# Kernel optimization log

Hardware: AMD Instinct MI355X
Metric: run time of the kernel (lower is better)

The kernel has to match this reference:

```python
import jax, jax.numpy as jnp
import numpy as np
import math

K_HEADS = 16  # nb_heads from init_kwargs


def setup_inputs() -> dict:
    key = jax.random.key(0)
    ks = jax.random.split(key, 7)
    B, M, H, D = 2, 2048, 1024, 1024 // K_HEADS
    return {
        "h": jax.random.normal(ks[0], (B, M, H), jnp.float32),
        "h_cache": jax.random.normal(ks[1], (B, M, H), jnp.float32),
        "key_pe": jax.random.normal(ks[2], (1, D, M), jnp.float32),
        "Wq": jax.random.normal(ks[3], (H, H), jnp.float32) * 0.02,
        "Wk": jax.random.normal(ks[4], (H, H), jnp.float32) * 0.02,
        "Wv": jax.random.normal(ks[5], (H, H), jnp.float32) * 0.02,
        "Wo": jax.random.normal(ks[6], (H, H), jnp.float32) * 0.02,
    }


def _heads(x, K):
    # [B, M, H] -> [B, K, M, D]
    B, M, H = x.shape
    return x.reshape(B, M, K, H // K).transpose(0, 2, 1, 3)


def reference(h, h_cache, key_pe, Wq, Wk, Wv, Wo):
    B, M, H = h.shape
    K = K_HEADS
    D = H // K
    q = _heads(h @ Wq.T, K)        # [B, K, M, D]
    k = _heads(h_cache @ Wk.T, K)  # [B, K, L, D], L == M
    v = _heads(h_cache @ Wv.T, K)  # [B, K, L, D]

    attn_cont = jnp.einsum("bkmd,bkld->bkml", q, k)            # content scores
    attn_pos = jnp.einsum("bkmd,dl->bkml", q, key_pe[0])       # positional scores
    attn = (attn_cont + attn_pos[..., :M]) / math.sqrt(D)
    attn = jax.nn.softmax(attn, axis=-1)  # computed as in source, but source
    # (faithfully) multiplies VALUE by attn_cont, not attn:
    out = jnp.einsum("bkml,bkld->bkmd", attn_cont, v)          # [B, K, M, D]
    out = out.transpose(0, 2, 1, 3).reshape(B, M, H)
    return out @ Wo.T
```

## Files before the change

### kernel.cpp

```cpp
#include <hip/hip_runtime.h>
#include <hip/hip_bf16.h>

#define BB 2
#define MM 2048
#define HH 1024
#define KH 16

typedef short s16x8 __attribute__((ext_vector_type(8)));
typedef float f32x4 __attribute__((ext_vector_type(4)));
typedef float f32x16 __attribute__((ext_vector_type(16)));

#define GLOBAL_AS __attribute__((address_space(1)))
#define LDS_AS    __attribute__((address_space(3)))

__device__ __forceinline__ void async_copy16(const void* g, void* l) {
    __builtin_amdgcn_global_load_lds((const GLOBAL_AS void*)g, (LDS_AS void*)l, 16, 0, 0);
}

struct __align__(8) bf16x4_t { __hip_bfloat16 x, y, z, w; };

__global__ __launch_bounds__(256) void cvt_all(
    const float* __restrict__ h_f, const float* __restrict__ hc_f,
    const float* __restrict__ Wk_f, const float* __restrict__ Wv_f,
    const float* __restrict__ Wo_f, const float* __restrict__ Wq_f,
    __hip_bfloat16* __restrict__ hb, __hip_bfloat16* __restrict__ hcT,
    __hip_bfloat16* __restrict__ wkb, __hip_bfloat16* __restrict__ wvb,
    __hip_bfloat16* __restrict__ wob, __hip_bfloat16* __restrict__ wqt,
    float* __restrict__ Sz)
{
    __shared__ float Tl[64][65];
    const int seg = blockIdx.y;
    const int t = threadIdx.x;
    const int bx = blockIdx.x;

    if (seg == 1) {
        if (bx >= BB * 512) return;
        const int b = bx >> 9;
        const int tile = bx & 511;
        const int m0 = (tile >> 4) * 64;
        const int k0 = (tile & 15) * 64;
        const int r = t >> 6;
        const int c = t & 63;
        const float* src = hc_f + (size_t)b * MM * HH;
#pragma unroll
        for (int i = 0; i < 64; i += 4)
            Tl[r + i][c] = src[(size_t)(m0 + r + i) * HH + k0 + c];
        __syncthreads();
        __hip_bfloat16* dst = hcT + (size_t)b * HH * MM;
        const int ml = (t & 15) * 4;
#pragma unroll
        for (int ii = 0; ii < 4; ++ii) {
            const int kl = (t >> 4) + 16 * ii;
            bf16x4_t o;
            o.x = __float2bfloat16(Tl[ml + 0][kl]);
            o.y = __float2bfloat16(Tl[ml + 1][kl]);
            o.z = __float2bfloat16(Tl[ml + 2][kl]);
            o.w = __float2bfloat16(Tl[ml + 3][kl]);
            *(bf16x4_t*)(dst + (size_t)(k0 + kl) * MM + m0 + ml) = o;
        }
        return;
    }
    if (seg == 5) {
        if (bx < 128) {
            const int i = (bx * 256 + t) * 4;
            float4 z = {0.f, 0.f, 0.f, 0.f};
            *(float4*)(Sz + i) = z;
            return;
        }
        if (bx >= 384) return;
        const int tile = bx - 128;
        const int j0 = (tile >> 4) * 64;
        const int k0 = (tile & 15) * 64;
        const int r = t >> 6;
        const int c = t & 63;
#pragma unroll
        for (int i = 0; i < 64; i += 4)
            Tl[r + i][c] = Wq_f[(size_t)(j0 + r + i) * HH + k0 + c];
        __syncthreads();
        const int ml = (t & 15) * 4;
#pragma unroll
        for (int ii = 0; ii < 4; ++ii) {
            const int kl = (t >> 4) + 16 * ii;
            bf16x4_t o;
            o.x = __float2bfloat16(Tl[ml + 0][kl]);
            o.y = __float2bfloat16(Tl[ml + 1][kl]);
            o.z = __float2bfloat16(Tl[ml + 2][kl]);
            o.w = __float2bfloat16(Tl[ml + 3][kl]);
            *(bf16x4_t*)(wqt + (size_t)(k0 + kl) * HH + j0 + ml) = o;
        }
        return;
    }
    const float* src;
    __hip_bfloat16* dst;
    int n;
    switch (seg) {
        case 0: src = h_f;  dst = hb;  n = BB * MM * HH; break;
        case 2: src = Wk_f; dst = wkb; n = HH * HH; break;
        case 3: src = Wv_f; dst = wvb; n = HH * HH; break;
        default: src = Wo_f; dst = wob; n = HH * HH; break;
    }
    const int i = (bx * 256 + t) * 4;
    if (i + 3 < n) {
        const float4 v = *(const float4*)(src + i);
        bf16x4_t o;
        o.x = __float2bfloat16(v.x);
        o.y = __float2bfloat16(v.y);
        o.z = __float2bfloat16(v.z);
        o.w = __float2bfloat16(v.w);
        *(bf16x4_t*)(dst + i) = o;
    }
}

__device__ __forceinline__ void store_c(__hip_bfloat16* C, size_t idx, float v) {
    C[idx] = __float2bfloat16(v);
}
__device__ __forceinline__ void store_c(float* C, size_t idx, float v) { C[idx] = v; }

__device__ __forceinline__ f32x16 nt64_acc(
    const __hip_bfloat16* __restrict__ A, const __hip_bfloat16* __restrict__ B,
    int kd, size_t ld, __hip_bfloat16* As, __hip_bfloat16* Bs)
{
    const int t    = threadIdx.x;
    const int lane = t & 63;
    const int wave = t >> 6;
    const int srow = lane >> 3;
    const int sw   = ((lane & 7) ^ srow) * 8;
    const int wm   = (wave >> 1) * 32;
    const int wn   = (wave & 1) * 32;
    const int fm   = lane & 31;
    const int fm7  = fm & 7;
    const int ghi  = lane >> 5;

    f32x16 acc = {};
    for (int k0 = 0; k0 < kd; k0 += 64) {
        __syncthreads();
#pragma unroll
        for (int i = 0; i < 2; ++i) {
            const int c = wave * 2 + i;
            async_copy16(A + (size_t)(c * 8 + srow) * ld + k0 + sw, As + c * 512);
            async_copy16(B + (size_t)(c * 8 + srow) * ld + k0 + sw, Bs + c * 512);
        }
        __syncthreads();
#pragma unroll
        for (int ks = 0; ks < 64; ks += 16) {
            const int pos = ((((ks >> 3) + ghi) ^ fm7) * 8);
            const s16x8 af = *(const s16x8*)(As + (wm + fm) * 64 + pos);
            const s16x8 bf = *(const s16x8*)(Bs + (wn + fm) * 64 + pos);
            acc = __builtin_amdgcn_mfma_f32_32x32x16_bf16(af, bf, acc, 0, 0, 0);
        }
    }
    return acc;
}

template <typename OutT>
__device__ __forceinline__ void store_tile64(OutT* C, int ldc, const f32x16& acc) {
    const int lane = threadIdx.x & 63;
    const int wave = threadIdx.x >> 6;
    const int wm = (wave >> 1) * 32;
    const int wn = (wave & 1) * 32;
    const int col = wn + (lane & 31);
    const int rb  = 4 * (lane >> 5);
#pragma unroll
    for (int r = 0; r < 16; ++r) {
        const int row = wm + (r & 3) + 8 * (r >> 2) + rb;
        store_c(C, (size_t)row * ldc + col, acc[r]);
    }
}

__global__ __launch_bounds__(256) void gemm_g(
    const __hip_bfloat16* __restrict__ hcT, __hip_bfloat16* __restrict__ G)
{
    __shared__ __align__(16) __hip_bfloat16 As[64 * 64];
    __shared__ __align__(16) __hip_bfloat16 Bs[64 * 64];
    const int b = blockIdx.z;
    const int m0 = blockIdx.x * 64, n0 = blockIdx.y * 64;
    const __hip_bfloat16* Ab = hcT + (size_t)b * HH * MM;
    f32x16 acc = nt64_acc(Ab + (size_t)m0 * MM, Ab + (size_t)n0 * MM, MM, MM, As, Bs);
    store_tile64(G + (size_t)b * HH * HH + (size_t)m0 * HH + n0, HH, acc);
}

#define LPP 72

__global__ __launch_bounds__(256) void gemm_vt(
    const __hip_bfloat16* __restrict__ wkb, const __hip_bfloat16* __restrict__ wvb,
    const __hip_bfloat16* __restrict__ G, float* __restrict__ S)
{
    __shared__ __align__(16) char smem[64 * LPP * 2 + 64 * 64 * 2];
    __hip_bfloat16* As = (__hip_bfloat16*)smem;
    __hip_bfloat16* Bs = (__hip_bfloat16*)(smem + 8192);
    __hip_bfloat16* Pl = (__hip_bfloat16*)smem;
    __hip_bfloat16* Wl = (__hip_bfloat16*)(smem + 64 * LPP * 2);

    const int t    = threadIdx.x;
    const int lane = t & 63;
    const int wave = t >> 6;
    const int kt   = blockIdx.x;
    const int head = blockIdx.y;
    const int b    = blockIdx.z;

    const __hip_bfloat16* Arow = G + (size_t)b * HH * HH + (size_t)kt * 64 * HH;
    const __hip_bfloat16* Brow = wkb + (size_t)head * 64 * HH;

    f32x16 acc = nt64_acc(Arow, Brow, HH, HH, As, Bs);
    __syncthreads();

    {
        const int wm = (wave >> 1) * 32;
        const int wn = (wave & 1) * 32;
        const int col_i = wn + (lane & 31);
        const int ghi4  = 4 * (lane >> 5);
#pragma unroll
        for (int g = 0; g < 4; ++g) {
            const int ccb = wm + 8 * g + ghi4;
            bf16x4_t o;
            o.x = __float2bfloat16(acc[4 * g + 0]);
            o.y = __float2bfloat16(acc[4 * g + 1]);
            o.z = __float2bfloat16(acc[4 * g + 2]);
            o.w = __float2bfloat16(acc[4 * g + 3]);
            *(bf16x4_t*)(Pl + col_i * LPP + ccb) = o;
        }
    }
    {
        const int srow = lane >> 3;
        const int sw   = ((lane & 7) ^ srow) * 8;
#pragma unroll
        for (int i = 0; i < 2; ++i) {
            const int c = wave * 2 + i;
            async_copy16(wvb + (size_t)(head * 64 + c * 8 + srow) * HH + kt * 64 + sw,
                         Wl + c * 512);
        }
    }
    __syncthreads();

    const int fr  = lane & 15;
    const int fq  = (lane >> 4) * 8;
    const int wm2 = wave * 16;

    f32x4 acc2[4] = {};
#pragma unroll
    for (int kk = 0; kk < 64; kk += 32) {
        const s16x8 af = *(const s16x8*)(Pl + (wm2 + fr) * LPP + kk + fq);
#pragma unroll
        for (int nj = 0; nj < 4; ++nj) {
            const int row = nj * 16 + fr;
            const s16x8 bfv = *(const s16x8*)(
                Wl + row * 64 + ((((kk + fq) >> 3) ^ (row & 7)) << 3));
            acc2[nj] = __builtin_amdgcn_mfma_f32_16x16x32_bf16(af, bfv, acc2[nj], 0, 0, 0);
        }
    }

    float* Sg = S + ((size_t)b * KH + head) * 4096;
    const int er = (lane >> 4) * 4;
    const int ec = lane & 15;
#pragma unroll
    for (int nj = 0; nj < 4; ++nj)
#pragma unroll
        for (int rr = 0; rr < 4; ++rr)
            atomicAdd(&Sg[(wm2 + er + rr) * 64 + nj * 16 + ec], acc2[nj][rr]);
}

__global__ __launch_bounds__(256) void gemm_f(
    const __hip_bfloat16* __restrict__ W2, const __hip_bfloat16* __restrict__ WqT,
    __hip_bfloat16* __restrict__ F)
{
    __shared__ __align__(16) __hip_bfloat16 As[64 * 64];
    __shared__ __align__(16) __hip_bfloat16 Bs[64 * 64];
    const int b = blockIdx.z;
    const int m0 = blockIdx.x * 64, n0 = blockIdx.y * 64;
    f32x16 acc = nt64_acc(W2 + (size_t)b * HH * HH + (size_t)m0 * HH,
                          WqT + (size_t)n0 * HH, HH, HH, As, Bs);
    store_tile64(F + (size_t)b * HH * HH + (size_t)m0 * HH + n0, HH, acc);
}

template <typename OutT>
__device__ __forceinline__ void gemm_nt_body64(
    const __hip_bfloat16* __restrict__ A,
    const __hip_bfloat16* __restrict__ Bm,
    OutT* __restrict__ C,
    __hip_bfloat16* As, __hip_bfloat16* Bs,
    int m0, int n0)
{
    const int t    = threadIdx.x;
    const int lane = t & 63;
    const int wave = t >> 6;

    const int srow = lane >> 3;
    const int sw   = ((lane & 7) ^ srow) * 8;

    const int wn  = wave * 32;
    const int fm  = lane & 31;
    const int fm7 = fm & 7;
    const int ghi = lane >> 5;

    f32x16 acc[2] = {};

    for (int k0 = 0; k0 < HH; k0 += 64) {
        __syncthreads();
        {
            const __hip_bfloat16* ag = A + (size_t)(m0 + wave * 16 + srow) * HH + k0 + sw;
            async_copy16(ag,          As + wave * 1024);
            async_copy16(ag + 8 * HH, As + wave * 1024 + 512);
        }
#pragma unroll
        for (int i = 0; i < 2; ++i) {
            const int c = wave * 2 + i;
            const __hip_bfloat16* bg = Bm + (size_t)(n0 + c * 16 + srow) * HH + k0 + sw;
            async_copy16(bg,          Bs + c * 1024);
            async_copy16(bg + 8 * HH, Bs + c * 1024 + 512);
        }
        __syncthreads();

#pragma unroll
        for (int ks = 0; ks < 64; ks += 16) {
            const int pos = ((((ks >> 3) + ghi) ^ fm7) * 8);
            s16x8 af[2], bf;
#pragma unroll
            for (int mi = 0; mi < 2; ++mi)
                af[mi] = *(const s16x8*)(As + (mi * 32 + fm) * 64 + pos);
            bf = *(const s16x8*)(Bs + (wn + fm) * 64 + pos);
#pragma unroll
            for (int mi = 0; mi < 2; ++mi)
                acc[mi] = __builtin_amdgcn_mfma_f32_32x32x16_bf16(
                    af[mi], bf, acc[mi], 0, 0, 0);
        }
    }

    const int ec = lane & 31;
    const int eb = (lane >> 5) * 4;
#pragma unroll
    for (int mi = 0; mi < 2; ++mi)
#pragma unroll
        for (int r = 0; r < 16; ++r) {
            const int m = m0 + mi * 32 + (r & 3) + 8 * (r >> 2) + eb;
            const int n = n0 + wn + ec;
            store_c(C, (size_t)m * HH + n, acc[mi][r]);
        }
}

__global__ __launch_bounds__(256) void gemm_final(
    const __hip_bfloat16* __restrict__ hb, const __hip_bfloat16* __restrict__ F,
    float* __restrict__ outg)
{
    __shared__ __align__(16) __hip_bfloat16 As[64 * 64];
    __shared__ __align__(16) __hip_bfloat16 Bs[128 * 64];
    const int b = blockIdx.z;
    gemm_nt_body64<float>(hb + (size_t)b * MM * HH, F + (size_t)b * HH * HH,
                          outg + (size_t)b * MM * HH, As, Bs,
                          blockIdx.x * 64, blockIdx.y * 128);
}

__global__ __launch_bounds__(256) void w2_fold(
    const __hip_bfloat16* __restrict__ Wo,
    const float* __restrict__ S,
    __hip_bfloat16* __restrict__ W2)
{
    __shared__ float Sl[64 * 68];
    __shared__ float Wl[128 * 68];
    const int t = threadIdx.x, head = blockIdx.y, b = blockIdx.z;
    const int n0 = blockIdx.x * 128;

    const float* Sg = S + ((size_t)b * KH + head) * 4096;
    for (int idx = t; idx < 4096; idx += 256) {
        const int dp = idx >> 6, d = idx & 63;
        Sl[d * 68 + dp] = Sg[idx];
    }
    for (int idx = t; idx < 1024; idx += 256) {
        const int r = idx >> 3, c8 = (idx & 7) * 8;
        s16x8 wv = *(const s16x8*)(Wo + (size_t)(n0 + r) * HH + head * 64 + c8);
#pragma unroll
        for (int j = 0; j < 8; ++j) {
            __hip_bfloat16 wb = *(((const __hip_bfloat16*)&wv) + j);
            Wl[r * 68 + c8 + j] = __bfloat162float(wb);
        }
    }
    __syncthreads();

    const int dpb = (t & 15) * 4;
    const int ng  = t >> 4;
    float acc[8][4] = {};
    for (int d0 = 0; d0 < 64; d0 += 4) {
        f32x4 sv[4];
#pragma unroll
        for (int r = 0; r < 4; ++r)
            sv[r] = *(const f32x4*)(Sl + (d0 + r) * 68 + dpb);
#pragma unroll
        for (int i = 0; i < 8; ++i) {
            const f32x4 wv = *(const f32x4*)(Wl + (ng + 16 * i) * 68 + d0);
#pragma unroll
            for (int r = 0; r < 4; ++r)
#pragma unroll
                for (int j = 0; j < 4; ++j)
                    acc[i][j] += wv[r] * sv[r][j];
        }
    }

#pragma unroll
    for (int i = 0; i < 8; ++i) {
        bf16x4_t o;
        o.x = __float2bfloat16(acc[i][0]);
        o.y = __float2bfloat16(acc[i][1]);
        o.z = __float2bfloat16(acc[i][2]);
        o.w = __float2bfloat16(acc[i][3]);
        *(bf16x4_t*)(W2 + (size_t)b * HH * HH + (size_t)(n0 + ng + 16 * i) * HH
                     + head * 64 + dpb) = o;
    }
}

extern "C" void kernel_launch(void* const* d_in, const int* in_sizes, int n_in,
                              void* d_out, int out_size, void* d_ws, size_t ws_size,
                              hipStream_t stream) {
    const float* h_f  = (const float*)d_in[0];
    const float* hc_f = (const float*)d_in[1];
    const float* Wq_f = (const float*)d_in[3];
    const float* Wk_f = (const float*)d_in[4];
    const float* Wv_f = (const float*)d_in[5];
    const float* Wo_f = (const float*)d_in[6];
    float* out = (float*)d_out;

    const size_t act_b = (size_t)BB * MM * HH * 2;
    const size_t w_b   = (size_t)HH * HH * 2;
    char* ws = (char*)d_ws;
    __hip_bfloat16* hb   = (__hip_bfloat16*)(ws);
    __hip_bfloat16* hcT  = (__hip_bfloat16*)(ws + act_b);
    __hip_bfloat16* wkb  = (__hip_bfloat16*)(ws + 2 * act_b);
    __hip_bfloat16* wvb  = (__hip_bfloat16*)(ws + 2 * act_b + w_b);
    __hip_bfloat16* wob  = (__hip_bfloat16*)(ws + 2 * act_b + 2 * w_b);
    __hip_bfloat16* wqt  = (__hip_bfloat16*)(ws + 2 * act_b + 3 * w_b);
    __hip_bfloat16* Gb   = (__hip_bfloat16*)(ws + 2 * act_b + 4 * w_b);
    float*          Sbuf = (float*)(ws + 2 * act_b + 6 * w_b);
    __hip_bfloat16* W2   = (__hip_bfloat16*)(ws + 2 * act_b + 6 * w_b + (size_t)512 * 1024);
    __hip_bfloat16* Fbuf = (__hip_bfloat16*)(ws + 2 * act_b + 8 * w_b + (size_t)512 * 1024);

    const dim3 blk(256);

    cvt_all<<<dim3(4096, 6), blk, 0, stream>>>(h_f, hc_f, Wk_f, Wv_f, Wo_f, Wq_f,
                                               hb, hcT, wkb, wvb, wob, wqt, Sbuf);

    gemm_g<<<dim3(16, 16, BB), blk, 0, stream>>>(hcT, Gb);

    gemm_vt<<<dim3(16, KH, BB), blk, 0, stream>>>(wkb, wvb, Gb, Sbuf);

    w2_fold<<<dim3(8, KH, BB), blk, 0, stream>>>(wob, Sbuf, W2);

    gemm_f<<<dim3(16, 16, BB), blk, 0, stream>>>(W2, wqt, Fbuf);

    gemm_final<<<dim3(32, 8, BB), blk, 0, stream>>>(hb, Fbuf, out);
}
```

Before: 177.3 us.

## Exploit Gram symmetry, double K-step per sync, and use 64x64 tiles for final GEMM

The Gram GEMM G = hcT·hcTᵀ now computes only the upper-triangular 64x64 tiles (136 per batch). It mirrors each off-diagonal tile through LDS as a transposed store, which roughly halves its MFMA work and input reads. The shared NT accumulator stages two 64-wide K chunks per barrier pair, halving synchronizations at the cost of doubling LDS to 32KB per block. The final GEMM switches from 64x128 tiles to 64x64 tiles with twice as many blocks, trading B-tile reuse for more parallelism.

```diff
diff --git a/kernel.cpp b/kernel.cpp
--- a/kernel.cpp
+++ b/kernel.cpp
@@ -116,7 +116,7 @@
 }
 __device__ __forceinline__ void store_c(float* C, size_t idx, float v) { C[idx] = v; }
 
-__device__ __forceinline__ f32x16 nt64_acc(
+__device__ __forceinline__ f32x16 nt64x2_acc(
     const __hip_bfloat16* __restrict__ A, const __hip_bfloat16* __restrict__ B,
     int kd, size_t ld, __hip_bfloat16* As, __hip_bfloat16* Bs)
 {
@@ -132,22 +132,28 @@
     const int ghi  = lane >> 5;
 
     f32x16 acc = {};
-    for (int k0 = 0; k0 < kd; k0 += 64) {
+    for (int k0 = 0; k0 < kd; k0 += 128) {
         __syncthreads();
 #pragma unroll
-        for (int i = 0; i < 2; ++i) {
-            const int c = wave * 2 + i;
-            async_copy16(A + (size_t)(c * 8 + srow) * ld + k0 + sw, As + c * 512);
-            async_copy16(B + (size_t)(c * 8 + srow) * ld + k0 + sw, Bs + c * 512);
-        }
+        for (int h = 0; h < 2; ++h)
+#pragma unroll
+            for (int i = 0; i < 2; ++i) {
+                const int c = wave * 2 + i;
+                async_copy16(A + (size_t)(c * 8 + srow) * ld + k0 + 64 * h + sw,
+                             As + h * 4096 + c * 512);
+                async_copy16(B + (size_t)(c * 8 + srow) * ld + k0 + 64 * h + sw,
+                             Bs + h * 4096 + c * 512);
+            }
         __syncthreads();
 #pragma unroll
-        for (int ks = 0; ks < 64; ks += 16) {
-            const int pos = ((((ks >> 3) + ghi) ^ fm7) * 8);
-            const s16x8 af = *(const s16x8*)(As + (wm + fm) * 64 + pos);
-            const s16x8 bf = *(const s16x8*)(Bs + (wn + fm) * 64 + pos);
-            acc = __builtin_amdgcn_mfma_f32_32x32x16_bf16(af, bf, acc, 0, 0, 0);
-        }
+        for (int h = 0; h < 2; ++h)
+#pragma unroll
+            for (int ks = 0; ks < 64; ks += 16) {
+                const int pos = ((((ks >> 3) + ghi) ^ fm7) * 8);
+                const s16x8 af = *(const s16x8*)(As + h * 4096 + (wm + fm) * 64 + pos);
+                const s16x8 bf = *(const s16x8*)(Bs + h * 4096 + (wn + fm) * 64 + pos);
+                acc = __builtin_amdgcn_mfma_f32_32x32x16_bf16(af, bf, acc, 0, 0, 0);
+            }
     }
     return acc;
 }
@@ -170,13 +176,55 @@
 __global__ __launch_bounds__(256) void gemm_g(
     const __hip_bfloat16* __restrict__ hcT, __hip_bfloat16* __restrict__ G)
 {
-    __shared__ __align__(16) __hip_bfloat16 As[64 * 64];
-    __shared__ __align__(16) __hip_bfloat16 Bs[64 * 64];
+    __shared__ __align__(16) char smem[32768];
+    __hip_bfloat16* As = (__hip_bfloat16*)smem;
+    __hip_bfloat16* Bs = (__hip_bfloat16*)(smem + 16384);
+    __hip_bfloat16* Ts = (__hip_bfloat16*)smem;
+
     const int b = blockIdx.z;
-    const int m0 = blockIdx.x * 64, n0 = blockIdx.y * 64;
+    int i = 0, rem = blockIdx.x;
+    while (rem >= 16 - i) { rem -= 16 - i; ++i; }
+    const int j = i + rem;
+    const int m0 = i * 64, n0 = j * 64;
+
     const __hip_bfloat16* Ab = hcT + (size_t)b * HH * MM;
-    f32x16 acc = nt64_acc(Ab + (size_t)m0 * MM, Ab + (size_t)n0 * MM, MM, MM, As, Bs);
-    store_tile64(G + (size_t)b * HH * HH + (size_t)m0 * HH + n0, HH, acc);
+    f32x16 acc = nt64x2_acc(Ab + (size_t)m0 * MM, Ab + (size_t)n0 * MM, MM, MM, As, Bs);
+
+    __hip_bfloat16* Gb = G + (size_t)b * HH * HH;
+    store_tile64(Gb + (size_t)m0 * HH + n0, HH, acc);
+
+    if (i == j) return;
+
+    __syncthreads();
+    {
+        const int lane = threadIdx.x & 63;
+        const int wave = threadIdx.x >> 6;
+        const int wm = (wave >> 1) * 32;
+        const int wn = (wave & 1) * 32;
+        const int col = wn + (lane & 31);
+        const int rb  = 4 * (lane >> 5);
+#pragma unroll
+        for (int r = 0; r < 16; ++r) {
+            const int row = wm + (r & 3) + 8 * (r >> 2) + rb;
+            Ts[row * 72 + col] = __float2bfloat16(acc[r]);
+        }
+    }
+    __syncthreads();
+    {
+        const int t = threadIdx.x;
+        const int rp = t >> 2;
+        const int c0 = (t & 3) * 16;
+        __hip_bfloat16* dst = Gb + (size_t)(n0 + rp) * HH + m0 + c0;
+#pragma unroll
+        for (int kk = 0; kk < 4; ++kk) {
+            bf16x4_t o;
+            o.x = Ts[(c0 + 4 * kk + 0) * 72 + rp];
+            o.y = Ts[(c0 + 4 * kk + 1) * 72 + rp];
+            o.z = Ts[(c0 + 4 * kk + 2) * 72 + rp];
+            o.w = Ts[(c0 + 4 * kk + 3) * 72 + rp];
+            *(bf16x4_t*)(dst + 4 * kk) = o;
+        }
+    }
 }
 
 #define LPP 72
@@ -185,9 +233,9 @@
     const __hip_bfloat16* __restrict__ wkb, const __hip_bfloat16* __restrict__ wvb,
     const __hip_bfloat16* __restrict__ G, float* __restrict__ S)
 {
-    __shared__ __align__(16) char smem[64 * LPP * 2 + 64 * 64 * 2];
+    __shared__ __align__(16) char smem[32768];
     __hip_bfloat16* As = (__hip_bfloat16*)smem;
-    __hip_bfloat16* Bs = (__hip_bfloat16*)(smem + 8192);
+    __hip_bfloat16* Bs = (__hip_bfloat16*)(smem + 16384);
     __hip_bfloat16* Pl = (__hip_bfloat16*)smem;
     __hip_bfloat16* Wl = (__hip_bfloat16*)(smem + 64 * LPP * 2);
 
@@ -201,7 +249,7 @@
     const __hip_bfloat16* Arow = G + (size_t)b * HH * HH + (size_t)kt * 64 * HH;
     const __hip_bfloat16* Brow = wkb + (size_t)head * 64 * HH;
 
-    f32x16 acc = nt64_acc(Arow, Brow, HH, HH, As, Bs);
+    f32x16 acc = nt64x2_acc(Arow, Brow, HH, HH, As, Bs);
     __syncthreads();
 
     {
@@ -263,90 +311,28 @@
     const __hip_bfloat16* __restrict__ W2, const __hip_bfloat16* __restrict__ WqT,
     __hip_bfloat16* __restrict__ F)
 {
-    __shared__ __align__(16) __hip_bfloat16 As[64 * 64];
-    __shared__ __align__(16) __hip_bfloat16 Bs[64 * 64];
+    __shared__ __align__(16) char smem[32768];
+    __hip_bfloat16* As = (__hip_bfloat16*)smem;
+    __hip_bfloat16* Bs = (__hip_bfloat16*)(smem + 16384);
     const int b = blockIdx.z;
     const int m0 = blockIdx.x * 64, n0 = blockIdx.y * 64;
-    f32x16 acc = nt64_acc(W2 + (size_t)b * HH * HH + (size_t)m0 * HH,
-                          WqT + (size_t)n0 * HH, HH, HH, As, Bs);
+    f32x16 acc = nt64x2_acc(W2 + (size_t)b * HH * HH + (size_t)m0 * HH,
+                            WqT + (size_t)n0 * HH, HH, HH, As, Bs);
     store_tile64(F + (size_t)b * HH * HH + (size_t)m0 * HH + n0, HH, acc);
-}
-
-template <typename OutT>
-__device__ __forceinline__ void gemm_nt_body64(
-    const __hip_bfloat16* __restrict__ A,
-    const __hip_bfloat16* __restrict__ Bm,
-    OutT* __restrict__ C,
-    __hip_bfloat16* As, __hip_bfloat16* Bs,
-    int m0, int n0)
-{
-    const int t    = threadIdx.x;
-    const int lane = t & 63;
-    const int wave = t >> 6;
-
-    const int srow = lane >> 3;
-    const int sw   = ((lane & 7) ^ srow) * 8;
-
-    const int wn  = wave * 32;
-    const int fm  = lane & 31;
-    const int fm7 = fm & 7;
-    const int ghi = lane >> 5;
-
-    f32x16 acc[2] = {};
-
-    for (int k0 = 0; k0 < HH; k0 += 64) {
-        __syncthreads();
-        {
-            const __hip_bfloat16* ag = A + (size_t)(m0 + wave * 16 + srow) * HH + k0 + sw;
-            async_copy16(ag,          As + wave * 1024);
-            async_copy16(ag + 8 * HH, As + wave * 1024 + 512);
-        }
-#pragma unroll
-        for (int i = 0; i < 2; ++i) {
-            const int c = wave * 2 + i;
-            const __hip_bfloat16* bg = Bm + (size_t)(n0 + c * 16 + srow) * HH + k0 + sw;
-            async_copy16(bg,          Bs + c * 1024);
-            async_copy16(bg + 8 * HH, Bs + c * 1024 + 512);
-        }
-        __syncthreads();
-
-#pragma unroll
-        for (int ks = 0; ks < 64; ks += 16) {
-            const int pos = ((((ks >> 3) + ghi) ^ fm7) * 8);
-            s16x8 af[2], bf;
-#pragma unroll
-            for (int mi = 0; mi < 2; ++mi)
-                af[mi] = *(const s16x8*)(As + (mi * 32 + fm) * 64 + pos);
-            bf = *(const s16x8*)(Bs + (wn + fm) * 64 + pos);
-#pragma unroll
-            for (int mi = 0; mi < 2; ++mi)
-                acc[mi] = __builtin_amdgcn_mfma_f32_32x32x16_bf16(
-                    af[mi], bf, acc[mi], 0, 0, 0);
-        }
-    }
-
-    const int ec = lane & 31;
-    const int eb = (lane >> 5) * 4;
-#pragma unroll
-    for (int mi = 0; mi < 2; ++mi)
-#pragma unroll
-        for (int r = 0; r < 16; ++r) {
-            const int m = m0 + mi * 32 + (r & 3) + 8 * (r >> 2) + eb;
-            const int n = n0 + wn + ec;
-            store_c(C, (size_t)m * HH + n, acc[mi][r]);
-        }
 }
 
 __global__ __launch_bounds__(256) void gemm_final(
     const __hip_bfloat16* __restrict__ hb, const __hip_bfloat16* __restrict__ F,
     float* __restrict__ outg)
 {
-    __shared__ __align__(16) __hip_bfloat16 As[64 * 64];
-    __shared__ __align__(16) __hip_bfloat16 Bs[128 * 64];
+    __shared__ __align__(16) char smem[32768];
+    __hip_bfloat16* As = (__hip_bfloat16*)smem;
+    __hip_bfloat16* Bs = (__hip_bfloat16*)(smem + 16384);
     const int b = blockIdx.z;
-    gemm_nt_body64<float>(hb + (size_t)b * MM * HH, F + (size_t)b * HH * HH,
-                          outg + (size_t)b * MM * HH, As, Bs,
-                          blockIdx.x * 64, blockIdx.y * 128);
+    const int m0 = blockIdx.x * 64, n0 = blockIdx.y * 64;
+    f32x16 acc = nt64x2_acc(hb + (size_t)b * MM * HH + (size_t)m0 * HH,
+                            F + (size_t)b * HH * HH + (size_t)n0 * HH, HH, HH, As, Bs);
+    store_tile64(outg + (size_t)b * MM * HH + (size_t)m0 * HH + n0, HH, acc);
 }
 
 __global__ __launch_bounds__(256) void w2_fold(
@@ -436,7 +422,7 @@
     cvt_all<<<dim3(4096, 6), blk, 0, stream>>>(h_f, hc_f, Wk_f, Wv_f, Wo_f, Wq_f,
                                                hb, hcT, wkb, wvb, wob, wqt, Sbuf);
 
-    gemm_g<<<dim3(16, 16, BB), blk, 0, stream>>>(hcT, Gb);
+    gemm_g<<<dim3(136, 1, BB), blk, 0, stream>>>(hcT, Gb);
 
     gemm_vt<<<dim3(16, KH, BB), blk, 0, stream>>>(wkb, wvb, Gb, Sbuf);
 
@@ -444,5 +430,5 @@
 
     gemm_f<<<dim3(16, 16, BB), blk, 0, stream>>>(W2, wqt, Fbuf);
 
-    gemm_final<<<dim3(32, 8, BB), blk, 0, stream>>>(hb, Fbuf, out);
-}
+    gemm_final<<<dim3(32, 16, BB), blk, 0, stream>>>(hb, Fbuf, out);
+}
```

Result: faster. 169.1 us (-4.6%).
